# Performance work log

Measured on AMD Instinct MI355X. Metric: run time of the kernel, lower is better.

## Reference

```python
import jax, jax.numpy as jnp
import numpy as np

EPS = 1e-5

def binarize(x):
    # sign() forward with hardtanh straight-through estimator (1w1a BNN standard)
    c = jnp.clip(x, -1.0, 1.0)
    return c + jax.lax.stop_gradient(jnp.sign(x) - c)

def conv3x3(x, w):
    # NCHW 3x3 conv, stride 1, padding 1 (equivalent to ZeroPad2d(1) + 9 shifted 1x1 partial-sum convs)
    return jax.lax.conv_general_dilated(x, w, (1, 1), ((1, 1), (1, 1)),
                                        dimension_numbers=('NCHW', 'OIHW', 'NCHW'))

def bconv3x3(x, w):
    return conv3x3(binarize(x), binarize(w))

def bn(x, g, b):
    # training-mode BatchNorm2d with batch statistics
    m = jnp.mean(x, axis=(0, 2, 3), keepdims=True)
    v = jnp.var(x, axis=(0, 2, 3), keepdims=True)
    return (x - m) * jax.lax.rsqrt(v + EPS) * g[None, :, None, None] + b[None, :, None, None]

def maxpool2(x):
    return jax.lax.reduce_window(x, -jnp.inf, jax.lax.max, (1, 1, 2, 2), (1, 1, 2, 2), 'VALID')

hardtanh = lambda x: jnp.clip(x, -1.0, 1.0)

def setup_inputs() -> dict:
    key = jax.random.key(0)
    ks = jax.random.split(key, 10)
    d = {}
    d['x'] = jax.random.normal(ks[0], (256, 3, 32, 32), dtype=jnp.float32)
    shapes = [(128, 3), (128, 128), (256, 128), (256, 256), (512, 256), (512, 512)]
    for i, (co, ci) in enumerate(shapes):
        fan_in = ci * 9
        d[f'w{i}'] = jax.random.normal(ks[i + 1], (co, ci, 3, 3), dtype=jnp.float32) * np.float32((2.0 / fan_in) ** 0.5)
        d[f'g{i}'] = jnp.ones((co,), dtype=jnp.float32)
        d[f'b{i}'] = jnp.zeros((co,), dtype=jnp.float32)
    d['wfc'] = jax.random.normal(ks[7], (10, 8192), dtype=jnp.float32) * np.float32(8192 ** -0.5)
    d['bfc'] = jnp.zeros((10,), dtype=jnp.float32)
    return d

def reference(x, w0, g0, b0, w1, g1, b1, w2, g2, b2, w3, g3, b3,
              w4, g4, b4, w5, g5, b5, wfc, bfc):
    # conv0: full precision stem
    h = bn(conv3x3(x, w0), g0, b0)
    # binary blocks (1-bit weights and activations)
    h = hardtanh(bn(maxpool2(bconv3x3(h, w1)), g1, b1))
    h = hardtanh(bn(bconv3x3(h, w2), g2, b2))
    h = hardtanh(bn(maxpool2(bconv3x3(h, w3)), g3, b3))
    h = hardtanh(bn(bconv3x3(h, w4), g4, b4))
    h = hardtanh(bn(maxpool2(bconv3x3(h, w5)), g5, b5))
    h = h.reshape(h.shape[0], -1)  # [N, 512*4*4]
    return h @ wfc.T + bfc
```

## Files before the change

kernel.cpp:

```cpp
#include <hip/hip_runtime.h>
#include <cstdint>
#include <cstddef>

using u64 = unsigned long long;
using i64 = long long;

#define DEVI __device__ __forceinline__

DEVI double waveRed(double v) {
    #pragma unroll
    for (int o = 32; o > 0; o >>= 1) v += __shfl_down(v, o, 64);
    return v;
}

__global__ __launch_bounds__(256, 1) void conv0_sums3(const float* __restrict__ x,
                                                      const float* __restrict__ w0,
                                                      double* __restrict__ sum,
                                                      double* __restrict__ sumsq) {
    __shared__ float xs[3072];
    __shared__ float wsh[864];
    __shared__ double redS[4][32], redS2[4][32];
    int tid = threadIdx.x, n = blockIdx.y, co0 = blockIdx.x * 32;
    for (int i = tid; i < 3072; i += 256) xs[i] = x[n * 3072 + i];
    for (int i = tid; i < 864; i += 256) {
        int co = i / 27, j = i % 27;
        int ci = j % 3, k = j / 3;
        wsh[i] = w0[(co0 + co) * 27 + ci * 9 + k];
    }
    __syncthreads();

    float xv[4][27];
    #pragma unroll
    for (int k = 0; k < 4; ++k) {
        int pos = tid + k * 256, h = pos >> 5, w = pos & 31;
        #pragma unroll
        for (int kh = 0; kh < 3; ++kh) {
            #pragma unroll
            for (int kw = 0; kw < 3; ++kw) {
                #pragma unroll
                for (int ci = 0; ci < 3; ++ci) {
                    int ih = h + kh - 1, iw = w + kw - 1;
                    bool ok = (unsigned)ih < 32u && (unsigned)iw < 32u;
                    xv[k][(kh * 3 + kw) * 3 + ci] = ok ? xs[ci * 1024 + ih * 32 + iw] : 0.0f;
                }
            }
        }
    }
    int lane = tid & 63, wv = tid >> 6;
    for (int co = 0; co < 32; ++co) {
        #pragma clang fp contract(off)
        const float* wp = &wsh[co * 27];
        float a0 = 0.f, a1 = 0.f, a2 = 0.f, a3 = 0.f;
        #pragma unroll
        for (int j = 0; j < 27; ++j) {
            float wj = wp[j];
            a0 = __builtin_fmaf(xv[0][j], wj, a0);
            a1 = __builtin_fmaf(xv[1][j], wj, a1);
            a2 = __builtin_fmaf(xv[2][j], wj, a2);
            a3 = __builtin_fmaf(xv[3][j], wj, a3);
        }
        double y0 = a0, y1 = a1, y2 = a2, y3 = a3;
        double s  = (y0 + y1) + (y2 + y3);
        double s2 = (y0 * y0 + y1 * y1) + (y2 * y2 + y3 * y3);
        s = waveRed(s); s2 = waveRed(s2);
        if (lane == 0) { redS[wv][co] = s; redS2[wv][co] = s2; }
    }
    __syncthreads();
    if (tid < 32) {
        atomicAdd(&sum[co0 + tid], (redS[0][tid] + redS[1][tid]) + (redS[2][tid] + redS[3][tid]));
    } else if (tid < 64) {
        int c = tid - 32;
        atomicAdd(&sumsq[co0 + c], (redS2[0][c] + redS2[1][c]) + (redS2[2][c] + redS2[3][c]));
    }
}

__global__ void finalize_c0(const double* __restrict__ sum, const double* __restrict__ sumsq,
                            const float* __restrict__ g, const float* __restrict__ b,
                            double* __restrict__ M, double* __restrict__ A,
                            double* __restrict__ BB) {
    int c = threadIdx.x;
    double m = sum[c] / 262144.0;
    double var = sumsq[c] / 262144.0 - m * m;
    M[c]  = m;
    A[c]  = (double)g[c] / sqrt(var + 1e-5);
    BB[c] = (double)b[c];
}

__global__ __launch_bounds__(256, 1) void conv0_pack3(const float* __restrict__ x,
                                                      const float* __restrict__ w0,
                                                      const double* __restrict__ M,
                                                      const double* __restrict__ A,
                                                      const double* __restrict__ BB,
                                                      u64* __restrict__ A0) {
    __shared__ float xs[3072];
    __shared__ float wsh[3456];
    __shared__ double msh[128], ash[128], bsh[128];
    int tid = threadIdx.x, n = blockIdx.x >> 2;
    int pos = ((blockIdx.x & 3) << 8) + tid;
    for (int i = tid; i < 3072; i += 256) xs[i] = x[n * 3072 + i];
    for (int i = tid; i < 3456; i += 256) {
        int co = i / 27, j = i % 27;
        int ci = j % 3, k = j / 3;
        wsh[i] = w0[co * 27 + ci * 9 + k];
    }
    if (tid < 128) { msh[tid] = M[tid]; ash[tid] = A[tid]; bsh[tid] = BB[tid]; }
    __syncthreads();

    int h = pos >> 5, w = pos & 31;
    float xv[27];
    #pragma unroll
    for (int kh = 0; kh < 3; ++kh) {
        #pragma unroll
        for (int kw = 0; kw < 3; ++kw) {
            #pragma unroll
            for (int ci = 0; ci < 3; ++ci) {
                int ih = h + kh - 1, iw = w + kw - 1;
                bool ok = (unsigned)ih < 32u && (unsigned)iw < 32u;
                xv[(kh * 3 + kw) * 3 + ci] = ok ? xs[ci * 1024 + ih * 32 + iw] : 0.0f;
            }
        }
    }
    u64 b0 = 0, b1 = 0;
    #pragma unroll 4
    for (int co = 0; co < 128; ++co) {
        #pragma clang fp contract(off)
        float acc = 0.f;
        const float* wp = &wsh[co * 27];
        #pragma unroll
        for (int j = 0; j < 27; ++j) acc = __builtin_fmaf(xv[j], wp[j], acc);
        double t = ash[co] * ((double)acc - msh[co]) + bsh[co];
        u64 bit = t > 0.0 ? 1ull : 0ull;
        if (co < 64) b0 |= bit << co; else b1 |= bit << (co - 64);
    }
    size_t p = (size_t)n * 1024 + pos;
    A0[p * 2] = b0; A0[p * 2 + 1] = b1;
}

__global__ __launch_bounds__(256) void pack_w(const float* __restrict__ w,
                                              u64* __restrict__ Wb, int Ci, int Co) {
    int widx = blockIdx.x * 4 + (threadIdx.x >> 6);
    int lane = threadIdx.x & 63;
    int CW = Ci >> 6;
    int co = widx % Co;
    int rest = widx / Co;
    int cw = rest % CW;
    int k = rest / CW;
    int kh = k / 3, kw = k % 3;
    int ci = (cw << 6) | lane;
    float v = w[((size_t)(co * Ci + ci) * 3 + kh) * 3 + kw];
    u64 m = __ballot(v > 0.0f);
    if (lane == 0) Wb[widx] = m;
}

template <int CW, int CO, int HI, bool POOL>
__global__ __launch_bounds__(256, 2) void bconv_lds(const u64* __restrict__ A,
                                                    const u64* __restrict__ Wb,
                                                    short* __restrict__ dots,
                                                    i64* __restrict__ sums) {
    constexpr int WI = HI;
    constexpr int HO = POOL ? HI / 2 : HI;
    constexpr int WO = HO;
    constexpr int NR = POOL ? 4 : 3;
    constexpr int NCOL = POOL ? 4 : 3;
    constexpr int CPB = (CO < 256) ? CO : 256;
    constexpr int BPR = CO / CPB;
    constexpr int WSPLIT = 256 / CPB;
    constexpr int WOT = WO / WSPLIT;
    constexpr int CH = CW / 2;
    constexpr int LROW = (WI + 2) * CW;
    constexpr int NWORD = NR * LROW;
    constexpr int NC = POOL ? 4 : 1;

    __shared__ alignas(16) u64 xs[NWORD];

    const int tid = threadIdx.x;
    const int bid = blockIdx.x;
    const int coh = bid % BPR;
    const int rest = bid / BPR;
    const int ho = rest % HO;
    const int n = rest / HO;
    const int co = coh * CPB + (tid % CPB);
    const int wo0 = (tid / CPB) * WOT;
    const int hbase = POOL ? 2 * ho - 1 : ho - 1;

    const u64* An = A + (size_t)n * HI * WI * CW;
    for (int i = tid; i < NWORD; i += 256) {
        int r = i / LROW;
        int rem = i - r * LROW;
        int c = rem / CW;
        int ch = rem - c * CW;
        int ih = hbase + r, iw = c - 1;
        u64 v = 0;
        if ((unsigned)ih < (unsigned)HI && (unsigned)iw < (unsigned)WI)
            v = An[(size_t)(ih * WI + iw) * CW + ch];
        xs[i] = v;
    }
    __syncthreads();

    int q[WOT * NC];
    #pragma unroll
    for (int i = 0; i < WOT * NC; ++i) q[i] = 0;
    int P[9];
    #pragma unroll
    for (int k = 0; k < 9; ++k) P[k] = 0;

    const int c0 = POOL ? 2 * wo0 : wo0;

    #pragma unroll 1
    for (int ch2 = 0; ch2 < CH; ++ch2) {
        u64 wa[9], wb[9];
        #pragma unroll
        for (int k = 0; k < 9; ++k) {
            wa[k] = Wb[(size_t)(k * CW + 2 * ch2) * CO + co];
            wb[k] = Wb[(size_t)(k * CW + 2 * ch2 + 1) * CO + co];
        }
        #pragma unroll
        for (int k = 0; k < 9; ++k) P[k] += __popcll(wa[k]) + __popcll(wb[k]);

        u64 wx[NR][NCOL], wy[NR][NCOL];
        #pragma unroll
        for (int s = 0; s < 2; ++s) {
            #pragma unroll
            for (int r = 0; r < NR; ++r) {
                const ulonglong2 v = *(const ulonglong2*)&xs[r * LROW + (c0 + s) * CW + 2 * ch2];
                wx[r][s] = v.x; wy[r][s] = v.y;
            }
        }
        #pragma unroll
        for (int j = 0; j < WOT; ++j) {
            if constexpr (!POOL) {
                #pragma unroll
                for (int r = 0; r < NR; ++r) {
                    const ulonglong2 v = *(const ulonglong2*)&xs[r * LROW + (c0 + j + 2) * CW + 2 * ch2];
                    wx[r][(j + 2) % 3] = v.x; wy[r][(j + 2) % 3] = v.y;
                }
                int qq = 0;
                #pragma unroll
                for (int kh = 0; kh < 3; ++kh) {
                    #pragma unroll
                    for (int kw = 0; kw < 3; ++kw) {
                        const int sl = (j + kw) % 3;
                        qq += __popcll(wx[kh][sl] ^ wa[kh * 3 + kw])
                            + __popcll(wy[kh][sl] ^ wb[kh * 3 + kw]);
                    }
                }
                q[j] += qq;
            } else {
                #pragma unroll
                for (int s = 2; s < 4; ++s) {
                    const int sl = (2 * j + s) & 3;
                    #pragma unroll
                    for (int r = 0; r < NR; ++r) {
                        const ulonglong2 v = *(const ulonglong2*)&xs[r * LROW + (c0 + 2 * j + s) * CW + 2 * ch2];
                        wx[r][sl] = v.x; wy[r][sl] = v.y;
                    }
                }
                #pragma unroll
                for (int py = 0; py < 2; ++py) {
                    #pragma unroll
                    for (int px = 0; px < 2; ++px) {
                        int qq = 0;
                        #pragma unroll
                        for (int kh = 0; kh < 3; ++kh) {
                            #pragma unroll
                            for (int kw = 0; kw < 3; ++kw) {
                                const int sl = (2 * j + px + kw) & 3;
                                qq += __popcll(wx[py + kh][sl] ^ wa[kh * 3 + kw])
                                    + __popcll(wy[py + kh][sl] ^ wb[kh * 3 + kw]);
                            }
                        }
                        q[j * 4 + py * 2 + px] += qq;
                    }
                }
            }
        }
    }

    const int prT = P[0] + P[1] + P[2];
    const int prB = P[6] + P[7] + P[8];
    const int pcL = P[0] + P[3] + P[6];
    const int pcR = P[2] + P[5] + P[8];
    const int k00 = P[0], k02 = P[2], k20 = P[6], k22 = P[8];

    int accS = 0, accS2 = 0;
    #pragma unroll
    for (int j = 0; j < WOT; ++j) {
        const int wo = wo0 + j;
        int best;
        if constexpr (!POOL) {
            const int rT = (ho == 0), rB = (ho == HI - 1);
            const int cL = (wo == 0), cR = (wo == WI - 1);
            const int nv = (3 - rT - rB) * (3 - cL - cR);
            const int pad = (rT ? prT : 0) + (rB ? prB : 0) + (cL ? pcL : 0) + (cR ? pcR : 0)
                          - ((rT & cL) ? k00 : 0) - ((rT & cR) ? k02 : 0)
                          - ((rB & cL) ? k20 : 0) - ((rB & cR) ? k22 : 0);
            best = 64 * CW * nv + 2 * pad - 2 * q[j];
        } else {
            best = -(1 << 30);
            #pragma unroll
            for (int py = 0; py < 2; ++py) {
                #pragma unroll
                for (int px = 0; px < 2; ++px) {
                    const int hc = 2 * ho + py, wc = 2 * wo + px;
                    const int rT = (hc == 0), rB = (hc == HI - 1);
                    const int cL = (wc == 0), cR = (wc == WI - 1);
                    const int nv = (3 - rT - rB) * (3 - cL - cR);
                    const int pad = (rT ? prT : 0) + (rB ? prB : 0) + (cL ? pcL : 0) + (cR ? pcR : 0)
                                  - ((rT & cL) ? k00 : 0) - ((rT & cR) ? k02 : 0)
                                  - ((rB & cL) ? k20 : 0) - ((rB & cR) ? k22 : 0);
                    const int d = 64 * CW * nv + 2 * pad - 2 * q[j * 4 + py * 2 + px];
                    best = d > best ? d : best;
                }
            }
        }
        dots[(size_t)((n * HO + ho) * WO + wo) * CO + co] = (short)best;
        accS += best;
        accS2 += best * best;
    }
    atomicAdd((u64*)&sums[co], (u64)(i64)accS);
    atomicAdd((u64*)&sums[CO + co], (u64)(i64)accS2);
}

__global__ void finalize_bn(const i64* __restrict__ sums,
                            const float* __restrict__ g, const float* __restrict__ b,
                            int CO, double cnt, double* __restrict__ M,
                            double* __restrict__ A, double* __restrict__ BB) {
    int c = blockIdx.x * blockDim.x + threadIdx.x;
    if (c >= CO) return;
    double m = (double)sums[c] / cnt;
    double var = (double)sums[CO + c] / cnt - m * m;
    M[c]  = m;
    A[c]  = (double)g[c] / sqrt(var + 1e-5);
    BB[c] = (double)b[c];
}

template <int CO>
__global__ __launch_bounds__(256) void binpack_k(const short* __restrict__ xin,
                                                 const double* __restrict__ M,
                                                 const double* __restrict__ A,
                                                 const double* __restrict__ BB,
                                                 u64* __restrict__ Ab) {
    constexpr int CWo = CO / 64;
    int widx = blockIdx.x * 4 + (threadIdx.x >> 6);
    int lane = threadIdx.x & 63;
    int w = widx & (CWo - 1);
    int p = widx / CWo;
    int c = (w << 6) | lane;
    double t = A[c] * ((double)xin[(size_t)p * CO + c] - M[c]) + BB[c];
    u64 m = __ballot(t > 0.0);
    if (lane == 0) Ab[widx] = m;
}

__global__ __launch_bounds__(256) void fc_k(const short* __restrict__ x5,
                                            const double* __restrict__ M,
                                            const double* __restrict__ A,
                                            const double* __restrict__ BB,
                                            const float* __restrict__ wfc,
                                            const float* __restrict__ bfc,
                                            float* __restrict__ out) {
    int n = blockIdx.x / 10, k = blockIdx.x % 10;
    double acc = 0.0;
    for (int i = threadIdx.x; i < 8192; i += 256) {
        int c = i >> 4, hw = i & 15, h = hw >> 2, ww = hw & 3;
        double t = A[c] * ((double)x5[(size_t)((n * 4 + h) * 4 + ww) * 512 + c] - M[c]) + BB[c];
        t = t < -1.0 ? -1.0 : (t > 1.0 ? 1.0 : t);
        acc += t * (double)wfc[(size_t)k * 8192 + i];
    }
    acc = waveRed(acc);
    __shared__ double sd[4];
    if ((threadIdx.x & 63) == 0) sd[threadIdx.x >> 6] = acc;
    __syncthreads();
    if (threadIdx.x == 0)
        out[n * 10 + k] = (float)(sd[0] + sd[1] + sd[2] + sd[3] + (double)bfc[k]);
}

extern "C" void kernel_launch(void* const* d_in, const int* in_sizes, int n_in,
                              void* d_out, int out_size, void* d_ws, size_t ws_size,
                              hipStream_t stream) {
    (void)in_sizes; (void)n_in; (void)out_size; (void)ws_size;

    const float* x   = (const float*)d_in[0];
    const float* w0  = (const float*)d_in[1];
    const float* g0  = (const float*)d_in[2];
    const float* b0  = (const float*)d_in[3];
    const float* w1  = (const float*)d_in[4];
    const float* g1  = (const float*)d_in[5];
    const float* b1  = (const float*)d_in[6];
    const float* w2  = (const float*)d_in[7];
    const float* g2  = (const float*)d_in[8];
    const float* b2  = (const float*)d_in[9];
    const float* w3  = (const float*)d_in[10];
    const float* g3  = (const float*)d_in[11];
    const float* b3  = (const float*)d_in[12];
    const float* w4  = (const float*)d_in[13];
    const float* g4  = (const float*)d_in[14];
    const float* b4  = (const float*)d_in[15];
    const float* w5  = (const float*)d_in[16];
    const float* g5  = (const float*)d_in[17];
    const float* b5  = (const float*)d_in[18];
    const float* wfc = (const float*)d_in[19];
    const float* bfc = (const float*)d_in[20];
    float* out = (float*)d_out;

    char* ws = (char*)d_ws;
    double* sum0   = (double*)ws;
    double* sumsq0 = sum0 + 128;
    i64* isums = (i64*)(sumsq0 + 128);
    double* M  = (double*)(ws + 65536);
    double* A  = M + 3072;
    double* BB = A + 3072;
    char* p = ws + 65536 + 73728;
    u64* A0 = (u64*)p;  p += (size_t)262144 * 2 * 8;
    u64* A1 = (u64*)p;  p += (size_t)65536 * 2 * 8;
    u64* A2 = (u64*)p;  p += (size_t)65536 * 4 * 8;
    u64* A3 = (u64*)p;  p += (size_t)16384 * 4 * 8;
    u64* A4 = (u64*)p;  p += (size_t)16384 * 8 * 8;
    u64* Wb1 = (u64*)p; p += 2304 * 8;
    u64* Wb2 = (u64*)p; p += 4608 * 8;
    u64* Wb3 = (u64*)p; p += 9216 * 8;
    u64* Wb4 = (u64*)p; p += 18432 * 8;
    u64* Wb5 = (u64*)p; p += 36864 * 8;
    p = (char*)(((uintptr_t)p + 255) & ~(uintptr_t)255);
    short* dots = (short*)p;

    hipMemsetAsync(d_ws, 0, 43008, stream);

    pack_w<<<576,  256, 0, stream>>>(w1, Wb1, 128, 128);
    pack_w<<<1152, 256, 0, stream>>>(w2, Wb2, 128, 256);
    pack_w<<<2304, 256, 0, stream>>>(w3, Wb3, 256, 256);
    pack_w<<<4608, 256, 0, stream>>>(w4, Wb4, 256, 512);
    pack_w<<<9216, 256, 0, stream>>>(w5, Wb5, 512, 512);

    conv0_sums3<<<dim3(4, 256), 256, 0, stream>>>(x, w0, sum0, sumsq0);
    finalize_c0<<<1, 128, 0, stream>>>(sum0, sumsq0, g0, b0, M, A, BB);
    conv0_pack3<<<1024, 256, 0, stream>>>(x, w0, M, A, BB, A0);

    bconv_lds<2, 128, 32, true><<<4096, 256, 0, stream>>>(A0, Wb1, dots, isums);
    finalize_bn<<<1, 128, 0, stream>>>(isums, g1, b1, 128, 65536.0, M + 512, A + 512, BB + 512);
    binpack_k<128><<<32768, 256, 0, stream>>>(dots, M + 512, A + 512, BB + 512, A1);

    bconv_lds<2, 256, 16, false><<<4096, 256, 0, stream>>>(A1, Wb2, dots, isums + 1024);
    finalize_bn<<<1, 256, 0, stream>>>(isums + 1024, g2, b2, 256, 65536.0, M + 1024, A + 1024, BB + 1024);
    binpack_k<256><<<65536, 256, 0, stream>>>(dots, M + 1024, A + 1024, BB + 1024, A2);

    bconv_lds<4, 256, 16, true><<<2048, 256, 0, stream>>>(A2, Wb3, dots, isums + 2048);
    finalize_bn<<<1, 256, 0, stream>>>(isums + 2048, g3, b3, 256, 16384.0, M + 1536, A + 1536, BB + 1536);
    binpack_k<256><<<16384, 256, 0, stream>>>(dots, M + 1536, A + 1536, BB + 1536, A3);

    bconv_lds<4, 512, 8, false><<<4096, 256, 0, stream>>>(A3, Wb4, dots, isums + 3072);
    finalize_bn<<<1, 512, 0, stream>>>(isums + 3072, g4, b4, 512, 16384.0, M + 2048, A + 2048, BB + 2048);
    binpack_k<512><<<32768, 256, 0, stream>>>(dots, M + 2048, A + 2048, BB + 2048, A4);

    bconv_lds<8, 512, 8, true><<<2048, 256, 0, stream>>>(A4, Wb5, dots, isums + 4096);
    finalize_bn<<<1, 512, 0, stream>>>(isums + 4096, g5, b5, 512, 4096.0, M + 2560, A + 2560, BB + 2560);

    fc_k<<<2560, 256, 0, stream>>>(dots, M + 2560, A + 2560, BB + 2560, wfc, bfc, out);
}
```

Before: 913.3 us.

## Replace LDS-tiled binary conv with register-resident weight kernel for three layers

Adds a bconv_bits3 kernel where each thread owns one output channel and one output row. The thread keeps all 9*CW packed weight words in registers and reads activations straight from global memory (broadcast across the wave) instead of staging them in LDS. Three of the five binary conv layers are switched to it. This removes LDS staging and sync, but it adds high register pressure (up to 72 u64 for CW=8) and relies on cache hits for the activation reads.

```diff
diff --git a/kernel.cpp b/kernel.cpp
--- a/kernel.cpp
+++ b/kernel.cpp
@@ -153,13 +153,78 @@
 }
 
 template <int CW, int CO, int HI, bool POOL>
+__global__ __launch_bounds__(256, 2) void bconv_bits3(const u64* __restrict__ A,
+                                                      const u64* __restrict__ Wb,
+                                                      short* __restrict__ dots,
+                                                      i64* __restrict__ sums) {
+    constexpr int WI = HI;
+    constexpr int HO = POOL ? HI / 2 : HI;
+    constexpr int WO = HO;
+    int gid = blockIdx.x * 256 + threadIdx.x;
+    int co = gid % CO;
+    int rest = gid / CO;
+    int ho = rest % HO;
+    int n = rest / HO;
+
+    u64 wreg[9 * CW];
+    #pragma unroll
+    for (int t = 0; t < 9 * CW; ++t) wreg[t] = Wb[(size_t)t * CO + co];
+
+    const u64* An = A + (size_t)n * HI * WI * CW;
+    int s = 0, s2 = 0;
+    #pragma unroll 2
+    for (int wo = 0; wo < WO; ++wo) {
+        int best = -(1 << 30);
+        #pragma unroll
+        for (int py = 0; py < (POOL ? 2 : 1); ++py) {
+            #pragma unroll
+            for (int px = 0; px < (POOL ? 2 : 1); ++px) {
+                int hc = POOL ? 2 * ho + py : ho;
+                int wc = POOL ? 2 * wo + px : wo;
+                int pa[3], pb[3];
+                #pragma unroll
+                for (int k = 0; k < 3; ++k) { pa[k] = 0; pb[k] = 0; }
+                int nv = 0;
+                #pragma unroll
+                for (int kh = 0; kh < 3; ++kh) {
+                    int ih = hc + kh - 1;
+                    if ((unsigned)ih >= (unsigned)HI) continue;
+                    #pragma unroll
+                    for (int kw = 0; kw < 3; ++kw) {
+                        int iw = wc + kw - 1;
+                        if ((unsigned)iw >= (unsigned)WI) continue;
+                        const ulonglong2* ap =
+                            (const ulonglong2*)(An + (size_t)(ih * WI + iw) * CW);
+                        #pragma unroll
+                        for (int cw = 0; cw < CW / 2; ++cw) {
+                            ulonglong2 v = ap[cw];
+                            pa[kh] += __popcll(v.x ^ wreg[(kh * 3 + kw) * CW + 2 * cw]);
+                            pb[kh] += __popcll(v.y ^ wreg[(kh * 3 + kw) * CW + 2 * cw + 1]);
+                        }
+                        nv += CW * 64;
+                    }
+                }
+                int pc = (pa[0] + pa[1] + pa[2]) + (pb[0] + pb[1] + pb[2]);
+                int dot = nv - 2 * pc;
+                best = dot > best ? dot : best;
+            }
+        }
+        dots[(size_t)((n * HO + ho) * WO + wo) * CO + co] = (short)best;
+        s += best;
+        s2 += best * best;
+    }
+    atomicAdd((u64*)&sums[co], (u64)(i64)s);
+    atomicAdd((u64*)&sums[CO + co], (u64)(i64)s2);
+}
+
+template <int CW, int CO, int HI, bool POOL>
 __global__ __launch_bounds__(256, 2) void bconv_lds(const u64* __restrict__ A,
                                                     const u64* __restrict__ Wb,
                                                     short* __restrict__ dots,
                                                     i64* __restrict__ sums) {
     constexpr int WI = HI;
     constexpr int HO = POOL ? HI / 2 : HI;
-    constexpr int WO = HO;
+    constexpr int WO = POOL ? WI / 2 : WI;
     constexpr int NR = POOL ? 4 : 3;
     constexpr int NCOL = POOL ? 4 : 3;
     constexpr int CPB = (CO < 256) ? CO : 256;
@@ -439,7 +504,7 @@
     finalize_bn<<<1, 128, 0, stream>>>(isums, g1, b1, 128, 65536.0, M + 512, A + 512, BB + 512);
     binpack_k<128><<<32768, 256, 0, stream>>>(dots, M + 512, A + 512, BB + 512, A1);
 
-    bconv_lds<2, 256, 16, false><<<4096, 256, 0, stream>>>(A1, Wb2, dots, isums + 1024);
+    bconv_bits3<2, 256, 16, false><<<4096, 256, 0, stream>>>(A1, Wb2, dots, isums + 1024);
     finalize_bn<<<1, 256, 0, stream>>>(isums + 1024, g2, b2, 256, 65536.0, M + 1024, A + 1024, BB + 1024);
     binpack_k<256><<<65536, 256, 0, stream>>>(dots, M + 1024, A + 1024, BB + 1024, A2);
 
@@ -447,11 +512,11 @@
     finalize_bn<<<1, 256, 0, stream>>>(isums + 2048, g3, b3, 256, 16384.0, M + 1536, A + 1536, BB + 1536);
     binpack_k<256><<<16384, 256, 0, stream>>>(dots, M + 1536, A + 1536, BB + 1536, A3);
 
-    bconv_lds<4, 512, 8, false><<<4096, 256, 0, stream>>>(A3, Wb4, dots, isums + 3072);
+    bconv_bits3<4, 512, 8, false><<<4096, 256, 0, stream>>>(A3, Wb4, dots, isums + 3072);
     finalize_bn<<<1, 512, 0, stream>>>(isums + 3072, g4, b4, 512, 16384.0, M + 2048, A + 2048, BB + 2048);
     binpack_k<512><<<32768, 256, 0, stream>>>(dots, M + 2048, A + 2048, BB + 2048, A4);
 
-    bconv_lds<8, 512, 8, true><<<2048, 256, 0, stream>>>(A4, Wb5, dots, isums + 4096);
+    bconv_bits3<8, 512, 8, true><<<2048, 256, 0, stream>>>(A4, Wb5, dots, isums + 4096);
     finalize_bn<<<1, 512, 0, stream>>>(isums + 4096, g5, b5, 512, 4096.0, M + 2560, A + 2560, BB + 2560);
 
     fc_k<<<2560, 256, 0, stream>>>(dots, M + 2560, A + 2560, BB + 2560, wfc, bfc, out);
```

Result: slower. 1.041 ms (+14.0%).
